# Optimization experiments

Hardware: AMD Instinct MI355X
Metric: run time of the kernel (lower is better)

The kernel has to match this reference:

```python
import jax, jax.numpy as jnp
import numpy as np

D_MODEL = 1024
NUM_HEADS = 16


def setup_inputs() -> dict:
    key = jax.random.key(0)
    ks = jax.random.split(key, 11)
    B, L, D = 1, 4096, D_MODEL
    s = 1.0 / np.sqrt(D)
    inp = {
        "Q": jax.random.normal(ks[0], (B, L, D), jnp.float32),
        "K": jax.random.normal(ks[1], (B, L, D), jnp.float32),
        "V": jax.random.normal(ks[2], (B, L, D), jnp.float32),
        "w_q": jax.random.normal(ks[3], (D, D), jnp.float32) * s,
        "b_q": jax.random.normal(ks[4], (D,), jnp.float32) * s,
        "w_k": jax.random.normal(ks[5], (D, D), jnp.float32) * s,
        "b_k": jax.random.normal(ks[6], (D,), jnp.float32) * s,
        "w_v": jax.random.normal(ks[7], (D, D), jnp.float32) * s,
        "b_v": jax.random.normal(ks[8], (D,), jnp.float32) * s,
        "w_o": jax.random.normal(ks[9], (D, D), jnp.float32) * s,
        "b_o": jax.random.normal(ks[10], (D,), jnp.float32) * s,
    }
    return inp


def _split_heads(x, n_heads):
    B, L, D = x.shape
    return x.reshape(B, L, n_heads, D // n_heads).transpose(0, 2, 1, 3)  # (B,H,L,Dh)


def reference(Q, K, V, w_q, b_q, w_k, b_k, w_v, b_v, w_o, b_o):
    H = NUM_HEADS
    # QKV projections (torch Linear: x @ W.T + b)
    q = _split_heads(Q @ w_q.T + b_q, H)
    k = _split_heads(K @ w_k.T + b_k, H)
    v = _split_heads(V @ w_v.T + b_v, H)
    d_h = q.shape[-1]
    scores = jnp.einsum("bhqd,bhkd->bhqk", q, k) / jnp.sqrt(jnp.float32(d_h))
    attn = jax.nn.softmax(scores, axis=-1)
    out = jnp.einsum("bhqk,bhkd->bhqd", attn, v)  # (B,H,L,Dh)
    B, _, L, _ = out.shape
    out = out.transpose(0, 2, 1, 3).reshape(B, L, H * d_h)
    return out @ w_o.T + b_o
```

## Files before the change

### kernel.cpp

```cpp
#include <hip/hip_runtime.h>
#include <hip/hip_bf16.h>
#include <stdint.h>

#define D_MODEL 1024
#define NHEAD   16
#define DH      64

typedef __attribute__((ext_vector_type(8))) short bf16x8;
typedef __attribute__((ext_vector_type(4))) float f32x4;

__device__ __forceinline__ ushort f2bf(float f) {
    __hip_bfloat16 h = __float2bfloat16(f);
    return *reinterpret_cast<ushort*>(&h);
}

__device__ __forceinline__ void gload_lds16(const void* g, void* l) {
    __builtin_amdgcn_global_load_lds(
        (const __attribute__((address_space(1))) void*)g,
        (__attribute__((address_space(3))) void*)l, 16, 0, 0);
}

__device__ __forceinline__ bf16x8 load8f(const float* p) {
    const float4 a = *(const float4*)p;
    const float4 b = *(const float4*)(p + 4);
    bf16x8 r;
    r[0] = (short)f2bf(a.x); r[1] = (short)f2bf(a.y);
    r[2] = (short)f2bf(a.z); r[3] = (short)f2bf(a.w);
    r[4] = (short)f2bf(b.x); r[5] = (short)f2bf(b.y);
    r[6] = (short)f2bf(b.z); r[7] = (short)f2bf(b.w);
    return r;
}

__global__ __launch_bounds__(256) void cvt_w_kernel(
    const float* __restrict__ w0, const float* __restrict__ w1,
    const float* __restrict__ w2, const float* __restrict__ w3,
    ushort* __restrict__ out)
{
    const int g = blockIdx.x * 256 + threadIdx.x;
    const int m = g >> 17;
    const int off = (g & 131071) * 8;
    const float* src = (m == 0) ? w0 : (m == 1) ? w1 : (m == 2) ? w2 : w3;
    *(bf16x8*)(out + (size_t)m * 1048576 + off) = load8f(src + off);
}

__device__ __forceinline__ void storeC(float*  C, size_t i, float v) { C[i] = v; }
__device__ __forceinline__ void storeC(ushort* C, size_t i, float v) { C[i] = (short)f2bf(v); }

template<int NW, bool A_F32, typename TX, typename TOUT>
__device__ __forceinline__ void gemm_core(
    const TX* __restrict__ X,
    const ushort* __restrict__ Wb,
    const float* __restrict__ Bias,
    TOUT* __restrict__ C,
    int M, int N, int K, float scale,
    short* As, short* Bs)
{
    const int tid  = threadIdx.x;
    const int w    = tid >> 6;
    const int lane = tid & 63;
    const int quad = lane >> 4;
    const int l15  = lane & 15;
    const int wr   = (NW == 4) ? (w >> 1) : (w >> 2);
    const int wc   = (NW == 4) ? (w & 1)  : (w & 3);
    const int NJ   = (NW == 4) ? 4 : 2;
    const int colw = (NW == 4) ? 64 : 32;

    int bx = blockIdx.x, by = blockIdx.y;
    if (gridDim.x == 8 && (gridDim.y & 7) == 0) {
        const int fid   = by * 8 + bx;
        const int xcd   = fid & 7;
        const int local = fid >> 3;
        const int rpx   = gridDim.y >> 3;
        by = xcd * rpx + (local >> 3);
        bx = local & 7;
    }
    const int m0 = by * 128;
    const int n0 = bx * 128;

    f32x4 acc[4][4] = {};

    for (int k0 = 0; k0 < K; k0 += 32) {
        __syncthreads();
        #pragma unroll
        for (int c = 0; c < 8 / NW; ++c) {
            int chunk = w * (8 / NW) + c;
            int row   = chunk * 16 + (lane >> 2);
            gload_lds16(Wb + (size_t)(n0 + row) * K + k0 + (lane & 3) * 8,
                        &Bs[chunk * 512]);
        }
        if constexpr (A_F32) {
            #pragma unroll
            for (int c = 0; c < 2; ++c) {
                int idx = c * 256 + tid;
                int row = idx >> 2;
                int col = (idx & 3) * 8;
                *(bf16x8*)&As[row * 32 + col] =
                    load8f((const float*)X + (size_t)(m0 + row) * K + k0 + col);
            }
        } else {
            #pragma unroll
            for (int c = 0; c < 8 / NW; ++c) {
                int chunk = w * (8 / NW) + c;
                int row   = chunk * 16 + (lane >> 2);
                gload_lds16((const ushort*)X + (size_t)(m0 + row) * K + k0 + (lane & 3) * 8,
                            &As[chunk * 512]);
            }
        }
        __syncthreads();

        bf16x8 af[4], bfr[4];
        #pragma unroll
        for (int i = 0; i < 4; ++i)
            af[i] = *(const bf16x8*)&As[(wr * 64 + i * 16 + l15) * 32 + quad * 8];
        #pragma unroll
        for (int j = 0; j < NJ; ++j)
            bfr[j] = *(const bf16x8*)&Bs[(wc * colw + j * 16 + l15) * 32 + quad * 8];
        #pragma unroll
        for (int i = 0; i < 4; ++i)
            #pragma unroll
            for (int j = 0; j < NJ; ++j)
                acc[i][j] = __builtin_amdgcn_mfma_f32_16x16x32_bf16(af[i], bfr[j], acc[i][j], 0, 0, 0);
    }

    float bias[4];
    #pragma unroll
    for (int j = 0; j < NJ; ++j)
        bias[j] = Bias[n0 + wc * colw + j * 16 + l15];

    #pragma unroll
    for (int i = 0; i < 4; ++i) {
        int row = m0 + wr * 64 + i * 16 + quad * 4;
        #pragma unroll
        for (int j = 0; j < NJ; ++j) {
            int col = n0 + wc * colw + j * 16 + l15;
            #pragma unroll
            for (int r = 0; r < 4; ++r)
                storeC(C, (size_t)(row + r) * N + col, (acc[i][j][r] + bias[j]) * scale);
        }
    }
}

__global__ __launch_bounds__(256) void qkv_proj_kernel(
    const float* __restrict__ Qin, const float* __restrict__ Kin,
    const float* __restrict__ Vin,
    const ushort* __restrict__ Wb,
    const float* __restrict__ Bq, const float* __restrict__ Bk,
    const float* __restrict__ Bv,
    ushort* qo, ushort* ko, ushort* vo, int L)
{
    __shared__ short As[4096];
    __shared__ short Bs[4096];
    const int z = blockIdx.z;
    const float *X, *B; ushort* C;
    float scale = 1.0f;
    if (z == 0)      { X = Qin; B = Bq; C = qo; scale = 0.125f * 1.44269504088896f; }
    else if (z == 1) { X = Kin; B = Bk; C = ko; }
    else             { X = Vin; B = Bv; C = vo; }
    gemm_core<4, true, float, ushort>(X, Wb + (size_t)z * 1048576, B, C,
                                      L, D_MODEL, D_MODEL, scale, As, Bs);
}

__global__ __launch_bounds__(512) void out_proj_kernel(
    const ushort* __restrict__ Xa, const ushort* __restrict__ Wb,
    const float* __restrict__ Bo, float* out, int L)
{
    __shared__ short As[4096];
    __shared__ short Bs[4096];
    gemm_core<8, false, ushort, float>(Xa, Wb + (size_t)3 * 1048576, Bo, out,
                                       L, D_MODEL, D_MODEL, 1.0f, As, Bs);
}

__global__ __launch_bounds__(512) void attn_kernel(
    const ushort* __restrict__ Qw,
    const ushort* __restrict__ Kw,
    const ushort* __restrict__ Vw,
    ushort* __restrict__ Ow, int L)
{
    __shared__ short Ks[64 * 64];
    __shared__ short Vs[64 * 64];
    __shared__ short Ps[8][16 * 64];

    const int tid  = threadIdx.x;
    const int w    = tid >> 6;
    const int lane = tid & 63;
    const int quad = lane >> 4;
    const int l15  = lane & 15;
    const int h    = blockIdx.y;
    const int q0   = blockIdx.x * 128;

    const ushort* qp = Qw + (size_t)(q0 + w * 16 + l15) * D_MODEL + h * DH + quad * 8;
    bf16x8 qf0 = *(const bf16x8*)(qp);
    bf16x8 qf1 = *(const bf16x8*)(qp + 32);

    const int kkey = tid >> 3;
    const int kc8  = tid & 7;
    const int vkey = lane;
    const int vdh  = w * 8;

    const int krswz0 = ((quad    ) ^ (l15 & 7)) * 8;
    const int krswz1 = ((quad + 4) ^ (l15 & 7)) * 8;

    f32x4 o[4] = {};
    float m_run = -3e38f, l_run = 0.f;
    const float thr = 8.0f;

    const ushort* kptr = Kw + (size_t)kkey * D_MODEL + h * DH + kc8 * 8;
    const ushort* vptr = Vw + (size_t)vkey * D_MODEL + h * DH + vdh;
    bf16x8 kreg = *(const bf16x8*)kptr;
    bf16x8 vreg = *(const bf16x8*)vptr;

    for (int key0 = 0; key0 < L; key0 += 64) {
        __syncthreads();
        *(bf16x8*)&Ks[kkey * 64 + ((kc8 ^ (kkey & 7)) * 8)] = kreg;
        #pragma unroll
        for (int i = 0; i < 8; ++i)
            Vs[(vdh + i) * 64 + (((vkey >> 3) ^ i) * 8) + (vkey & 7)] = vreg[i];
        __syncthreads();

        if (key0 + 64 < L) {
            kptr += (size_t)64 * D_MODEL;
            vptr += (size_t)64 * D_MODEL;
            kreg = *(const bf16x8*)kptr;
            vreg = *(const bf16x8*)vptr;
        }

        f32x4 st[4];
        #pragma unroll
        for (int kt = 0; kt < 4; ++kt) {
            const int kr = (kt * 16 + l15) * 64;
            bf16x8 kf0 = *(const bf16x8*)&Ks[kr + krswz0];
            bf16x8 kf1 = *(const bf16x8*)&Ks[kr + krswz1];
            f32x4 z = {};
            z = __builtin_amdgcn_mfma_f32_16x16x32_bf16(kf0, qf0, z, 0, 0, 0);
            z = __builtin_amdgcn_mfma_f32_16x16x32_bf16(kf1, qf1, z, 0, 0, 0);
            st[kt] = z;
        }

        float mx = st[0][0];
        #pragma unroll
        for (int kt = 0; kt < 4; ++kt)
            #pragma unroll
            for (int r = 0; r < 4; ++r)
                mx = fmaxf(mx, st[kt][r]);
        mx = fmaxf(mx, __shfl_xor(mx, 16));
        mx = fmaxf(mx, __shfl_xor(mx, 32));

        if (!__all(mx <= m_run + thr)) {
            const float mnew  = fmaxf(m_run, mx);
            const float alpha = __builtin_amdgcn_exp2f(m_run - mnew);
            m_run = mnew;
            l_run *= alpha;
            float a[4];
            #pragma unroll
            for (int r = 0; r < 4; ++r)
                a[r] = __shfl(alpha, (lane & 48) | (quad * 4 + r));
            #pragma unroll
            for (int dt = 0; dt < 4; ++dt)
                #pragma unroll
                for (int r = 0; r < 4; ++r)
                    o[dt][r] *= a[r];
        }

        float rs = 0.f;
        #pragma unroll
        for (int kt = 0; kt < 4; ++kt) {
            float p0 = __builtin_amdgcn_exp2f(st[kt][0] - m_run);
            float p1 = __builtin_amdgcn_exp2f(st[kt][1] - m_run);
            float p2 = __builtin_amdgcn_exp2f(st[kt][2] - m_run);
            float p3 = __builtin_amdgcn_exp2f(st[kt][3] - m_run);
            rs += (p0 + p1) + (p2 + p3);
            uint2 pk;
            pk.x = (uint32_t)f2bf(p0) | ((uint32_t)f2bf(p1) << 16);
            pk.y = (uint32_t)f2bf(p2) | ((uint32_t)f2bf(p3) << 16);
            const int G = kt * 2 + (quad >> 1);
            *(uint2*)&Ps[w][l15 * 64 + ((G ^ (l15 & 7)) * 8) + (quad & 1) * 4] = pk;
        }
        rs += __shfl_xor(rs, 16);
        rs += __shfl_xor(rs, 32);
        l_run += rs;

        #pragma unroll
        for (int f = 0; f < 2; ++f) {
            bf16x8 pf = *(const bf16x8*)&Ps[w][l15 * 64 + (((f * 4 + quad) ^ (l15 & 7)) * 8)];
            #pragma unroll
            for (int dt = 0; dt < 4; ++dt) {
                bf16x8 vf = *(const bf16x8*)&Vs[(dt * 16 + l15) * 64 + (((f * 4 + quad) ^ (l15 & 7)) * 8)];
                o[dt] = __builtin_amdgcn_mfma_f32_16x16x32_bf16(pf, vf, o[dt], 0, 0, 0);
            }
        }
    }

    const float inv = 1.f / l_run;
    #pragma unroll
    for (int r = 0; r < 4; ++r) {
        const float linv = __shfl(inv, (lane & 48) | (quad * 4 + r));
        const int row = q0 + w * 16 + quad * 4 + r;
        #pragma unroll
        for (int dt = 0; dt < 4; ++dt) {
            int col = h * DH + dt * 16 + l15;
            Ow[(size_t)row * D_MODEL + col] = (short)f2bf(o[dt][r] * linv);
        }
    }
}

extern "C" void kernel_launch(void* const* d_in, const int* in_sizes, int n_in,
                              void* d_out, int out_size, void* d_ws, size_t ws_size,
                              hipStream_t stream) {
    const float* Q   = (const float*)d_in[0];
    const float* K   = (const float*)d_in[1];
    const float* V   = (const float*)d_in[2];
    const float* w_q = (const float*)d_in[3];
    const float* b_q = (const float*)d_in[4];
    const float* w_k = (const float*)d_in[5];
    const float* b_k = (const float*)d_in[6];
    const float* w_v = (const float*)d_in[7];
    const float* b_v = (const float*)d_in[8];
    const float* w_o = (const float*)d_in[9];
    const float* b_o = (const float*)d_in[10];
    float* out = (float*)d_out;

    const int L = in_sizes[0] / D_MODEL;
    const size_t mat = (size_t)L * D_MODEL;

    ushort* Wb   = (ushort*)d_ws;
    ushort* a_ws = (ushort*)d_ws + 4 * 1048576;
    ushort* v_ws = a_ws + mat;
    ushort* q_ws = (ushort*)d_out;
    ushort* k_ws = q_ws + mat;

    cvt_w_kernel<<<dim3(2048), dim3(256), 0, stream>>>(w_q, w_k, w_v, w_o, Wb);

    dim3 gqkv(D_MODEL / 128, L / 128, 3);
    qkv_proj_kernel<<<gqkv, dim3(256), 0, stream>>>(Q, K, V, Wb, b_q, b_k, b_v,
                                                    q_ws, k_ws, v_ws, L);
    dim3 gattn(L / 128, NHEAD);
    attn_kernel<<<gattn, dim3(512), 0, stream>>>(q_ws, k_ws, v_ws, a_ws, L);
    dim3 gout(D_MODEL / 128, L / 128);
    out_proj_kernel<<<gout, dim3(512), 0, stream>>>(a_ws, Wb, b_o, out, L);
}
```

Baseline: 301.8 us.

## Double GEMM K-tile to 64 with XOR-swizzled LDS layout

Changes the shared GEMM core used by the QKV and output projections to stage K tiles of 64 instead of 32, halving the number of barrier pairs per block. LDS rows are now 64 elements with an XOR swizzle on the 8-element column chunk to avoid bank conflicts on the fragment reads. LDS use per block doubles, which may reduce occupancy, and the swizzle adds index arithmetic.

New measurement: 304.7 us. No clear change (+0.9%).

```diff
diff --git a/kernel.cpp b/kernel.cpp
--- a/kernel.cpp
+++ b/kernel.cpp
@@ -77,49 +77,60 @@
     const int m0 = by * 128;
     const int n0 = bx * 128;
 
+    const int srow = lane >> 3;
+    const int scol = (lane & 7) ^ srow;
+
     f32x4 acc[4][4] = {};
 
-    for (int k0 = 0; k0 < K; k0 += 32) {
+    for (int k0 = 0; k0 < K; k0 += 64) {
         __syncthreads();
         #pragma unroll
-        for (int c = 0; c < 8 / NW; ++c) {
-            int chunk = w * (8 / NW) + c;
-            int row   = chunk * 16 + (lane >> 2);
-            gload_lds16(Wb + (size_t)(n0 + row) * K + k0 + (lane & 3) * 8,
+        for (int c = 0; c < 16 / NW; ++c) {
+            int chunk = w * (16 / NW) + c;
+            int row   = chunk * 8 + srow;
+            gload_lds16(Wb + (size_t)(n0 + row) * K + k0 + scol * 8,
                         &Bs[chunk * 512]);
         }
         if constexpr (A_F32) {
             #pragma unroll
-            for (int c = 0; c < 2; ++c) {
+            for (int c = 0; c < 4; ++c) {
                 int idx = c * 256 + tid;
-                int row = idx >> 2;
-                int col = (idx & 3) * 8;
-                *(bf16x8*)&As[row * 32 + col] =
-                    load8f((const float*)X + (size_t)(m0 + row) * K + k0 + col);
+                int row = idx >> 3;
+                int lc  = idx & 7;
+                int p   = lc ^ (row & 7);
+                *(bf16x8*)&As[row * 64 + p * 8] =
+                    load8f((const float*)X + (size_t)(m0 + row) * K + k0 + lc * 8);
             }
         } else {
             #pragma unroll
-            for (int c = 0; c < 8 / NW; ++c) {
-                int chunk = w * (8 / NW) + c;
-                int row   = chunk * 16 + (lane >> 2);
-                gload_lds16((const ushort*)X + (size_t)(m0 + row) * K + k0 + (lane & 3) * 8,
+            for (int c = 0; c < 16 / NW; ++c) {
+                int chunk = w * (16 / NW) + c;
+                int row   = chunk * 8 + srow;
+                gload_lds16((const ushort*)X + (size_t)(m0 + row) * K + k0 + scol * 8,
                             &As[chunk * 512]);
             }
         }
         __syncthreads();
 
-        bf16x8 af[4], bfr[4];
-        #pragma unroll
-        for (int i = 0; i < 4; ++i)
-            af[i] = *(const bf16x8*)&As[(wr * 64 + i * 16 + l15) * 32 + quad * 8];
-        #pragma unroll
-        for (int j = 0; j < NJ; ++j)
-            bfr[j] = *(const bf16x8*)&Bs[(wc * colw + j * 16 + l15) * 32 + quad * 8];
-        #pragma unroll
-        for (int i = 0; i < 4; ++i)
-            #pragma unroll
-            for (int j = 0; j < NJ; ++j)
-                acc[i][j] = __builtin_amdgcn_mfma_f32_16x16x32_bf16(af[i], bfr[j], acc[i][j], 0, 0, 0);
+        #pragma unroll
+        for (int kk = 0; kk < 2; ++kk) {
+            bf16x8 af[4], bfr[4];
+            #pragma unroll
+            for (int i = 0; i < 4; ++i) {
+                int row = wr * 64 + i * 16 + l15;
+                af[i] = *(const bf16x8*)&As[row * 64 + (((kk * 4 + quad) ^ (row & 7)) * 8)];
+            }
+            #pragma unroll
+            for (int j = 0; j < NJ; ++j) {
+                int row = wc * colw + j * 16 + l15;
+                bfr[j] = *(const bf16x8*)&Bs[row * 64 + (((kk * 4 + quad) ^ (row & 7)) * 8)];
+            }
+            #pragma unroll
+            for (int i = 0; i < 4; ++i)
+                #pragma unroll
+                for (int j = 0; j < NJ; ++j)
+                    acc[i][j] = __builtin_amdgcn_mfma_f32_16x16x32_bf16(af[i], bfr[j], acc[i][j], 0, 0, 0);
+        }
     }
 
     float bias[4];
@@ -148,8 +159,8 @@
     const float* __restrict__ Bv,
     ushort* qo, ushort* ko, ushort* vo, int L)
 {
-    __shared__ short As[4096];
-    __shared__ short Bs[4096];
+    __shared__ short As[8192];
+    __shared__ short Bs[8192];
     const int z = blockIdx.z;
     const float *X, *B; ushort* C;
     float scale = 1.0f;
@@ -164,8 +175,8 @@
     const ushort* __restrict__ Xa, const ushort* __restrict__ Wb,
     const float* __restrict__ Bo, float* out, int L)
 {
-    __shared__ short As[4096];
-    __shared__ short Bs[4096];
+    __shared__ short As[8192];
+    __shared__ short Bs[8192];
     gemm_core<8, false, ushort, float>(Xa, Wb + (size_t)3 * 1048576, Bo, out,
                                        L, D_MODEL, D_MODEL, 1.0f, As, Bs);
 }
```

## Pre-convert QKV activations to bf16 and raise wave priority around attention MFMAs

Applied to the files above, without the earlier changes.

Adds a separate kernel that converts the fp32 Q/K/V inputs to bf16 in workspace (when the workspace is large enough), so the QKV projection GEMM can use the bf16 load path instead of converting fp32 inside its tile loop. This is meant to cut in-loop conversion and global read bytes in the GEMM, at the cost of an extra launch and a full fp32 read plus bf16 write pass. The attention kernel also wraps its two MFMA sections in s_setprio to favour matrix-issuing waves. Whether the new path runs depends on ws_size reaching 40 MiB.

New measurement: 286.8 us. -5.0%, faster.

```diff
diff --git a/kernel.cpp b/kernel.cpp
--- a/kernel.cpp
+++ b/kernel.cpp
@@ -43,6 +43,18 @@
     *(bf16x8*)(out + (size_t)m * 1048576 + off) = load8f(src + off);
 }
 
+__global__ __launch_bounds__(256) void cvt_x_kernel(
+    const float* __restrict__ Q, const float* __restrict__ K,
+    const float* __restrict__ V,
+    ushort* __restrict__ Qb, ushort* __restrict__ Kb, ushort* __restrict__ Vb)
+{
+    const int z = blockIdx.z;
+    const float* src = (z == 0) ? Q : (z == 1) ? K : V;
+    ushort* dst = (z == 0) ? Qb : (z == 1) ? Kb : Vb;
+    const int off = (blockIdx.x * 256 + threadIdx.x) * 8;
+    *(bf16x8*)(dst + off) = load8f(src + off);
+}
+
 __device__ __forceinline__ void storeC(float*  C, size_t i, float v) { C[i] = v; }
 __device__ __forceinline__ void storeC(ushort* C, size_t i, float v) { C[i] = (short)f2bf(v); }
 
@@ -140,7 +152,7 @@
     }
 }
 
-__global__ __launch_bounds__(256) void qkv_proj_kernel(
+__global__ __launch_bounds__(256) void qkv_proj_f32_kernel(
     const float* __restrict__ Qin, const float* __restrict__ Kin,
     const float* __restrict__ Vin,
     const ushort* __restrict__ Wb,
@@ -160,6 +172,26 @@
                                       L, D_MODEL, D_MODEL, scale, As, Bs);
 }
 
+__global__ __launch_bounds__(256) void qkv_proj_bf16_kernel(
+    const ushort* __restrict__ Qb, const ushort* __restrict__ Kb,
+    const ushort* __restrict__ Vb,
+    const ushort* __restrict__ Wb,
+    const float* __restrict__ Bq, const float* __restrict__ Bk,
+    const float* __restrict__ Bv,
+    ushort* qo, ushort* ko, ushort* vo, int L)
+{
+    __shared__ short As[4096];
+    __shared__ short Bs[4096];
+    const int z = blockIdx.z;
+    const ushort *X; const float* B; ushort* C;
+    float scale = 1.0f;
+    if (z == 0)      { X = Qb; B = Bq; C = qo; scale = 0.125f * 1.44269504088896f; }
+    else if (z == 1) { X = Kb; B = Bk; C = ko; }
+    else             { X = Vb; B = Bv; C = vo; }
+    gemm_core<4, false, ushort, ushort>(X, Wb + (size_t)z * 1048576, B, C,
+                                        L, D_MODEL, D_MODEL, scale, As, Bs);
+}
+
 __global__ __launch_bounds__(512) void out_proj_kernel(
     const ushort* __restrict__ Xa, const ushort* __restrict__ Wb,
     const float* __restrict__ Bo, float* out, int L)
@@ -225,6 +257,7 @@
         }
 
         f32x4 st[4];
+        __builtin_amdgcn_s_setprio(1);
         #pragma unroll
         for (int kt = 0; kt < 4; ++kt) {
             const int kr = (kt * 16 + l15) * 64;
@@ -235,6 +268,7 @@
             z = __builtin_amdgcn_mfma_f32_16x16x32_bf16(kf1, qf1, z, 0, 0, 0);
             st[kt] = z;
         }
+        __builtin_amdgcn_s_setprio(0);
 
         float mx = st[0][0];
         #pragma unroll
@@ -279,6 +313,7 @@
         rs += __shfl_xor(rs, 32);
         l_run += rs;
 
+        __builtin_amdgcn_s_setprio(1);
         #pragma unroll
         for (int f = 0; f < 2; ++f) {
             bf16x8 pf = *(const bf16x8*)&Ps[w][l15 * 64 + (((f * 4 + quad) ^ (l15 & 7)) * 8)];
@@ -288,6 +323,7 @@
                 o[dt] = __builtin_amdgcn_mfma_f32_16x16x32_bf16(pf, vf, o[dt], 0, 0, 0);
             }
         }
+        __builtin_amdgcn_s_setprio(0);
     }
 
     const float inv = 1.f / l_run;
@@ -323,16 +359,35 @@
     const size_t mat = (size_t)L * D_MODEL;
 
     ushort* Wb   = (ushort*)d_ws;
-    ushort* a_ws = (ushort*)d_ws + 4 * 1048576;
-    ushort* v_ws = a_ws + mat;
     ushort* q_ws = (ushort*)d_out;
     ushort* k_ws = q_ws + mat;
+    const bool ext = ws_size >= (size_t)40 * 1024 * 1024;
+
+    ushort *a_ws, *v_ws, *Qb = nullptr, *Kb = nullptr, *Vb = nullptr;
+    if (ext) {
+        Vb   = (ushort*)d_ws + 4 * 1048576;
+        v_ws = Vb + mat;
+        Qb   = v_ws + mat;
+        Kb   = Qb + mat;
+        a_ws = Vb;
+    } else {
+        a_ws = (ushort*)d_ws + 4 * 1048576;
+        v_ws = a_ws + mat;
+    }
 
     cvt_w_kernel<<<dim3(2048), dim3(256), 0, stream>>>(w_q, w_k, w_v, w_o, Wb);
 
     dim3 gqkv(D_MODEL / 128, L / 128, 3);
-    qkv_proj_kernel<<<gqkv, dim3(256), 0, stream>>>(Q, K, V, Wb, b_q, b_k, b_v,
-                                                    q_ws, k_ws, v_ws, L);
+    if (ext) {
+        cvt_x_kernel<<<dim3(2048, 1, 3), dim3(256), 0, stream>>>(Q, K, V, Qb, Kb, Vb);
+        qkv_proj_bf16_kernel<<<gqkv, dim3(256), 0, stream>>>(Qb, Kb, Vb, Wb,
+                                                             b_q, b_k, b_v,
+                                                             q_ws, k_ws, v_ws, L);
+    } else {
+        qkv_proj_f32_kernel<<<gqkv, dim3(256), 0, stream>>>(Q, K, V, Wb,
+                                                            b_q, b_k, b_v,
+                                                            q_ws, k_ws, v_ws, L);
+    }
     dim3 gattn(L / 128, NHEAD);
     attn_kernel<<<gattn, dim3(512), 0, stream>>>(q_ws, k_ws, v_ws, a_ws, L);
     dim3 gout(D_MODEL / 128, L / 128);
```
